# Performance work log

Hardware: AMD Instinct MI355X
Metric: run time of the kernel (lower is better)

The kernel has to match this reference:

```python
import jax, jax.numpy as jnp
import numpy as np

IN_SIZE = 224
KERNEL = 5
STRIDE = 1
IN_CH = 16
OUT_CH = 64
LAMB = 5.0
LR = 0.005
GAMMA = 0.99
EPS_ = 0.01
NH = (IN_SIZE - KERNEL) // STRIDE + 1          # 220 output positions per side
NB_TILES = NH * NH                              # 48400 tiles


def setup_inputs() -> dict:
    key = jax.random.key(0)
    k1, k2 = jax.random.split(key)
    x = jax.random.normal(k1, (1, IN_CH, IN_SIZE, IN_SIZE), dtype=jnp.float32)
    # torch.nn.init.uniform_(param, a=0, b=1)
    W = jax.random.uniform(k2, (OUT_CH, IN_CH, KERNEL, KERNEL), dtype=jnp.float32)
    exp_avg = jnp.zeros((OUT_CH,), dtype=jnp.float32)
    return {"x": x, "W": W, "exp_avg": exp_avg, "clamped": 0}


def _inhibition(out):
    out = jax.nn.relu(out)
    m = jnp.max(out, axis=1, keepdims=True)     # max over channel dim
    out = out / (m + 1e-9)
    return out ** LAMB


def _flatten_input(x):
    # mirrors x.unfold(2,k,s).unfold(3,k,s) -> [T, C*k*k] with (C, kh, kw) ordering
    starts = jnp.arange(NH) * STRIDE
    rows = starts[:, None] + jnp.arange(KERNEL)  # [NH, K]
    p = x[0][:, rows]                            # [C, NH, K, W]
    p = p[:, :, :, rows]                         # [C, NH, K, NH, K]
    p = p.transpose(1, 3, 0, 2, 4)               # [NH, NH, C, K, K]
    return p.reshape(NB_TILES, -1)               # [T, D]


def reference(x, W, exp_avg, clamped):
    # forward conv + inhibition
    out = jax.lax.conv_general_dilated(
        x, W, (STRIDE, STRIDE), 'VALID',
        dimension_numbers=('NCHW', 'OIHW', 'NCHW'))
    out = _inhibition(out)                       # [1, O, NH, NH]

    # Hebbian FullyOrthogonal update (no-grad buffer update in the original)
    y = out[0].transpose(1, 2, 0).reshape(-1, OUT_CH)   # [T, O]
    xf = _flatten_input(x)                               # [T, D]
    Wf = W.reshape(OUT_CH, -1)                           # [O, D]
    # mean_t( lr * (y_t (x) x_t - y_t (x) (y_t W)) ) = lr/T * (Y^T X - (Y^T Y) W)
    yty = y.T @ y                                        # [O, O]
    avg_delta = (LR / NB_TILES) * (y.T @ xf - yty @ Wf)  # [O, D]
    Wnew = jax.nn.relu(Wf + avg_delta).reshape(OUT_CH, IN_CH, KERNEL, KERNEL)
    exp_new = GAMMA * exp_avg + (1.0 - GAMMA) * jnp.mean(y, axis=0)

    # weight decay scaling
    A = exp_new / jnp.mean(exp_new)
    gfp = EPS_ * jnp.tanh(-EPS_ * (A - 1.0)) + 1.0
    gfn = 1.0 / gfp
    pos = jnp.where(Wnew > 0, Wnew, 0.0) * gfp.reshape(-1, 1, 1, 1)
    neg = jnp.where(Wnew < 0, Wnew, 0.0) * gfn.reshape(-1, 1, 1, 1)
    Wfinal = pos + neg
    return out, Wfinal, exp_new
```

## Files before the change

kernel.cpp:

```cpp
#include <hip/hip_runtime.h>
#include <stdint.h>

#define IN_SIZE 224
#define KER 5
#define IN_CH 16
#define OUT_CH 64
#define NH 220
#define NB_TILES (NH * NH)
#define XCH (IN_SIZE * IN_SIZE)
#define OUT_PLANE NB_TILES
#define KP2 51200
#define XS 52224
#define LR_OVER_NB ((float)(0.005 / 48400.0))
#define GAMMA_F 0.99f
#define ONE_MINUS_GAMMA 0.01f
#define EPS_F 0.01f

#define NCHUNK 64
#define CK 800
#define PSTRIDE (64 * 512)

typedef __attribute__((ext_vector_type(8))) short short8;
typedef __attribute__((ext_vector_type(4))) float floatx4;

__device__ inline uint16_t f2bf(float f) {
    uint32_t u = __float_as_uint(f);
    return (uint16_t)((u + 0x7FFFu + ((u >> 16) & 1u)) >> 16);
}
__device__ inline float bf2f(uint16_t h) { return __uint_as_float((uint32_t)h << 16); }

__global__ __launch_bounds__(256) void prepa_kernel(const float* __restrict__ W,
                                                    uint16_t* __restrict__ wrh,
                                                    uint16_t* __restrict__ wrl) {
    int idx = blockIdx.x * 256 + threadIdx.x;
    if (idx >= 13 * 4 * 64 * 8) return;
    int j = idx & 7;
    int lane = (idx >> 3) & 63;
    int ocg = (idx >> 9) & 3;
    int t = idx >> 11;
    int k = (lane >> 4) * 8 + j;
    int s = k >> 4, c = k & 15;
    int oc = 16 * ocg + (lane & 15);
    int tap = 2 * t + s;
    float v = (tap < 25) ? W[oc * 400 + c * 25 + tap] : 0.f;
    uint16_t h = f2bf(v);
    wrh[idx] = h;
    wrl[idx] = f2bf(v - bf2f(h));
}

__global__ __launch_bounds__(256) void conv_prep_kernel(const uint16_t* __restrict__ wrh,
                                                        const uint16_t* __restrict__ wrl,
                                                        float* __restrict__ out,
                                                        uint16_t* __restrict__ yb,
                                                        const float* __restrict__ x,
                                                        uint16_t* __restrict__ xs,
                                                        uint16_t* __restrict__ ones) {
    if (blockIdx.x >= 770) {
        int t = (blockIdx.x - 770) * 256 + threadIdx.x;
        const int perq8 = XS / 8;
        {
            int kj = t / (16 * perq8);
            int rem = t - kj * (16 * perq8);
            int c = rem / perq8;
            int q = (rem - c * perq8) * 8;
            int base = c * XCH;
            uint32_t d[4];
#pragma unroll
            for (int p = 0; p < 4; p++) {
                int i0 = q + kj + 2 * p;
                int i1 = i0 + 1;
                uint16_t h0 = f2bf(x[base + (i0 < XCH ? i0 : XCH - 1)]);
                uint16_t h1 = f2bf(x[base + (i1 < XCH ? i1 : XCH - 1)]);
                d[p] = (uint32_t)h0 | ((uint32_t)h1 << 16);
            }
            *(uint4*)(xs + (kj * 16 + c) * XS + q) = make_uint4(d[0], d[1], d[2], d[3]);
        }
        ushort4 z = {0, 0, 0, 0};
        if (t < 64 * 480) {
            int r = t / 480, q = (t - r * 480) * 4;
            *(ushort4*)(yb + r * KP2 + 49280 + q) = z;
        }
        if (t < 64 * 220) {
            int o = t / 220, i = t - o * 220;
            *(ushort4*)(yb + o * KP2 + i * 224 + 220) = z;
        }
        if (t < 12816) {
            ushort4 o1 = {0x3F80, 0x3F80, 0x3F80, 0x3F80};
            ((ushort4*)ones)[t] = o1;
        }
        return;
    }

    const int lane = threadIdx.x & 63;
    const int w = threadIdx.x >> 6;
    const int l15 = lane & 15;
    const int quad = lane >> 4;
    const int P0 = blockIdx.x * 64;
    const int chalf = quad & 1;
    const int sq = quad >> 1;

    __shared__ uint16_t bsh[5 * 68 * 16];
    __shared__ uint16_t bsl[5 * 68 * 16];
    for (int u = threadIdx.x; u < 680; u += 256) {
        int row = u >> 1;
        int half = u & 1;
        int strip = row / 68;
        int rr = row - strip * 68;
        int grow = P0 + strip * 224 + rr;
        bool inb = grow < XCH;
        uint32_t dh[4], dl[4];
#pragma unroll
        for (int q = 0; q < 4; q++) {
            float v0 = inb ? x[(half * 8 + 2 * q) * XCH + grow] : 0.f;
            float v1 = inb ? x[(half * 8 + 2 * q + 1) * XCH + grow] : 0.f;
            uint16_t h0 = f2bf(v0), h1 = f2bf(v1);
            uint16_t l0 = f2bf(v0 - bf2f(h0)), l1 = f2bf(v1 - bf2f(h1));
            dh[q] = (uint32_t)h0 | ((uint32_t)h1 << 16);
            dl[q] = (uint32_t)l0 | ((uint32_t)l1 << 16);
        }
        int swz = (u ^ ((row >> 2) & 1)) * 8;
        *(uint4*)(bsh + swz) = make_uint4(dh[0], dh[1], dh[2], dh[3]);
        *(uint4*)(bsl + swz) = make_uint4(dl[0], dl[1], dl[2], dl[3]);
    }
    __syncthreads();

    floatx4 acc[4];
#pragma unroll
    for (int g = 0; g < 4; g++) acc[g] = (floatx4){0.f, 0.f, 0.f, 0.f};

#pragma unroll
    for (int t = 0; t < 13; t++) {
        short8 ah = *(const short8*)(wrh + ((t * 4 + w) * 64 + lane) * 8);
        short8 al = *(const short8*)(wrl + ((t * 4 + w) * 64 + lane) * 8);
        const int tap0 = 2 * t, tap1 = 2 * t + 1;
        const int ki0 = tap0 / 5, kj0 = tap0 % 5;
        const int ki1 = (tap1 <= 24) ? tap1 / 5 : 0;
        const int kj1 = (tap1 <= 24) ? tap1 % 5 : 0;
        const int strip = sq ? ki1 : ki0;
        const int kjv = sq ? kj1 : kj0;
#pragma unroll
        for (int g = 0; g < 4; g++) {
            int lrow = strip * 68 + 16 * g + l15 + kjv;
            int unit = lrow * 2 + chalf;
            int off = (unit ^ ((lrow >> 2) & 1)) * 8;
            short8 bh = *(const short8*)(bsh + off);
            short8 bl = *(const short8*)(bsl + off);
            acc[g] = __builtin_amdgcn_mfma_f32_16x16x32_bf16(ah, bh, acc[g], 0, 0, 0);
            acc[g] = __builtin_amdgcn_mfma_f32_16x16x32_bf16(ah, bl, acc[g], 0, 0, 0);
            acc[g] = __builtin_amdgcn_mfma_f32_16x16x32_bf16(al, bh, acc[g], 0, 0, 0);
        }
    }

    __shared__ float wmax[4][64];
    float pmax[4];
#pragma unroll
    for (int g = 0; g < 4; g++) {
        float mx = fmaxf(fmaxf(acc[g][0], acc[g][1]), fmaxf(acc[g][2], acc[g][3]));
        mx = fmaxf(mx, 0.f);
        mx = fmaxf(mx, __shfl_xor(mx, 16));
        mx = fmaxf(mx, __shfl_xor(mx, 32));
        pmax[g] = mx;
    }
    if (quad == 0) {
#pragma unroll
        for (int g = 0; g < 4; g++) wmax[w][g * 16 + l15] = pmax[g];
    }
    __syncthreads();

#pragma unroll
    for (int g = 0; g < 4; g++) {
        int P = P0 + 16 * g + l15;
        int i = P / 224;
        int j = P - i * 224;
        bool valid = j < NH;
        float mx = fmaxf(fmaxf(wmax[0][g * 16 + l15], wmax[1][g * 16 + l15]),
                         fmaxf(wmax[2][g * 16 + l15], wmax[3][g * 16 + l15]));
        float inv = 1.f / (mx + 1e-9f);
#pragma unroll
        for (int r = 0; r < 4; r++) {
            float tv = fmaxf(acc[g][r], 0.f) * inv;
            float t2 = tv * tv;
            tv = t2 * t2 * tv;
            if (valid) {
                int oc = 16 * w + quad * 4 + r;
                out[oc * OUT_PLANE + i * NH + j] = tv;
                yb[oc * KP2 + P] = f2bf(tv);
            }
        }
    }
}

__global__ __launch_bounds__(256) void gemm_kernel(const uint16_t* __restrict__ yb,
                                                   const uint16_t* __restrict__ xs,
                                                   const uint16_t* __restrict__ ones,
                                                   float* __restrict__ Mpart) {
    __shared__ uint16_t As[2][64 * 64];
    __shared__ uint16_t Bs[2][64 * 64];
    const int tid = threadIdx.x;
    const int lane = tid & 63;
    const int w = tid >> 6;
    const int l15 = lane & 15;
    const int quad = lane >> 4;
    const int b = blockIdx.x;
    const int xcd = b & 7;
    const int t8 = b >> 3;
    const int ntile = t8 & 7;
    const int chunk = xcd + 8 * (t8 >> 3);
    const int k0 = chunk * CK;

    const int sr = tid >> 2;
    const int sq = tid & 3;
    const int sseg = sq * 8;
    const uint16_t* pa = yb + sr * KP2 + k0 + sseg;

    int n_g = ntile * 64 + sr;
    const uint16_t* pbase;
    if (n_g < 400) {
        int c = n_g / 25;
        int r = n_g - 25 * c;
        int ki = r / 5;
        int kj = r - 5 * ki;
        pbase = xs + (kj * 16 + c) * XS + ki * 224;
    } else if (n_g < 464) {
        pbase = yb + (n_g - 400) * KP2;
    } else if (n_g == 464) {
        pbase = ones;
    } else {
        pbase = yb;
    }
    const uint16_t* pb = pbase + k0 + sseg;

    const int woff = sr * 64 + ((2 * sq + sr) & 7) * 8;
    const int ru = ((2 * quad + l15) & 7) * 8;
    floatx4 acc[4];
#pragma unroll
    for (int i = 0; i < 4; i++) acc[i] = (floatx4){0.f, 0.f, 0.f, 0.f};

    uint4 ra = *(const uint4*)pa;
    uint4 rb = *(const uint4*)pb;

    for (int s = 0; s < 25; s++) {
        const int p = s & 1;
        *(uint4*)&As[p][woff] = ra;
        *(uint4*)&Bs[p][woff] = rb;
        __syncthreads();
        if (s + 1 < 25) {
            pa += 32;
            pb += 32;
            ra = *(const uint4*)pa;
            rb = *(const uint4*)pb;
        }
        short8 af = *(const short8*)&As[p][(16 * w + l15) * 64 + ru];
#pragma unroll
        for (int ng = 0; ng < 4; ng++) {
            short8 bf = *(const short8*)&Bs[p][(16 * ng + l15) * 64 + ru];
            acc[ng] = __builtin_amdgcn_mfma_f32_16x16x32_bf16(af, bf, acc[ng], 0, 0, 0);
        }
        __syncthreads();
    }

    float* dst = Mpart + chunk * PSTRIDE;
#pragma unroll
    for (int ng = 0; ng < 4; ng++) {
        int col = ntile * 64 + ng * 16 + l15;
        if (col < 465) {
#pragma unroll
            for (int r = 0; r < 4; r++)
                dst[(16 * w + quad * 4 + r) * 512 + col] = acc[ng][r];
        }
    }
}

__global__ __launch_bounds__(256) void finalize_w_kernel(const float* __restrict__ W,
                                                         const float* __restrict__ Mpart,
                                                         const float* __restrict__ exp_avg,
                                                         float* __restrict__ Wout,
                                                         float* __restrict__ expout) {
    __shared__ float gfps[OUT_CH];
    __shared__ float ytys[2][OUT_CH];
    const int tid = threadIdx.x;
    const int bid = blockIdx.x;
    const int first_o = (bid * 256) / 400;

    if (tid < OUT_CH) {
        int o = tid;
        float cs = 0.f;
#pragma unroll 8
        for (int ch = 0; ch < NCHUNK; ch++) cs += Mpart[ch * PSTRIDE + o * 512 + 464];
        float e = GAMMA_F * exp_avg[o] + ONE_MINUS_GAMMA * (cs / (float)NB_TILES);
        float s = e;
        for (int off = 32; off; off >>= 1) s += __shfl_down(s, off);
        s = __shfl(s, 0);
        float A = e / (s / (float)OUT_CH);
        gfps[o] = EPS_F * tanhf(-EPS_F * (A - 1.f)) + 1.f;
        if (bid == 0) expout[o] = e;
    }
    if (tid >= 128) {
        int t = tid - 128;
        int orow = first_o + (t >> 6);
        int k = t & 63;
        float s = 0.f;
        if (orow < OUT_CH) {
#pragma unroll 8
            for (int ch = 0; ch < NCHUNK; ch++) s += Mpart[ch * PSTRIDE + orow * 512 + 400 + k];
        }
        ytys[t >> 6][k] = s;
    }
    __syncthreads();

    int idx = bid * 256 + tid;
    int o = idx / 400;
    int q = idx - o * 400;
    float Mv = 0.f;
#pragma unroll 8
    for (int ch = 0; ch < NCHUNK; ch++) Mv += Mpart[ch * PSTRIDE + o * 512 + q];
    const float* yrow = ytys[o - first_o];
    float dot = 0.f;
#pragma unroll 8
    for (int k = 0; k < OUT_CH; k++) dot = fmaf(yrow[k], W[k * 400 + q], dot);
    float wv = W[idx] + LR_OVER_NB * (Mv - dot);
    wv = fmaxf(wv, 0.f);
    float gp = gfps[o];
    float pos = (wv > 0.f ? wv : 0.f) * gp;
    float neg = (wv < 0.f ? wv : 0.f) / gp;
    Wout[idx] = pos + neg;
}

extern "C" void kernel_launch(void* const* d_in, const int* in_sizes, int n_in,
                              void* d_out, int out_size, void* d_ws, size_t ws_size,
                              hipStream_t stream) {
    const float* x = (const float*)d_in[0];
    const float* W = (const float*)d_in[1];
    const float* exp_avg = (const float*)d_in[2];
    float* out = (float*)d_out;

    float* wsf = (float*)d_ws;
    float* Mpart = wsf + 29760;
    uint16_t* wrh = (uint16_t*)Mpart;
    uint16_t* wrl = wrh + 26624;
    uint16_t* ybf = (uint16_t*)(wsf + 29760 + NCHUNK * PSTRIDE);
    uint16_t* xsb = ybf + OUT_CH * KP2;
    uint16_t* ones = xsb + 5 * 16 * XS;

    float* Wout = out + OUT_CH * OUT_PLANE;
    float* expout = Wout + OUT_CH * IN_CH * KER * KER;

    prepa_kernel<<<104, 256, 0, stream>>>(W, wrh, wrl);
    conv_prep_kernel<<<770 + 2040, 256, 0, stream>>>(wrh, wrl, out, ybf, x, xsb, ones);
    gemm_kernel<<<512, 256, 0, stream>>>(ybf, xsb, ones, Mpart);
    finalize_w_kernel<<<100, 256, 0, stream>>>(W, Mpart, exp_avg, Wout, expout);
}
```

Before: 112.7 us.

## Fuse weight split into conv kernel and atomically reduce GEMM partials

Drops the separate prepa_kernel launch. Each conv block now loads W directly and splits it into bf16 hi/lo register fragments. The GEMM kernel now atomically adds its per-chunk partial sums into one zeroed 64x512 buffer instead of writing 64 partial slabs. The finalize kernel then reads single values instead of summing 64 chunks. This trades one launch and a strided reduction for redundant per-block weight conversion (26 short8 registers per thread) and float atomic contention across 64 chunks.

```diff
diff --git a/kernel.cpp b/kernel.cpp
--- a/kernel.cpp
+++ b/kernel.cpp
@@ -29,32 +29,13 @@
 }
 __device__ inline float bf2f(uint16_t h) { return __uint_as_float((uint32_t)h << 16); }
 
-__global__ __launch_bounds__(256) void prepa_kernel(const float* __restrict__ W,
-                                                    uint16_t* __restrict__ wrh,
-                                                    uint16_t* __restrict__ wrl) {
-    int idx = blockIdx.x * 256 + threadIdx.x;
-    if (idx >= 13 * 4 * 64 * 8) return;
-    int j = idx & 7;
-    int lane = (idx >> 3) & 63;
-    int ocg = (idx >> 9) & 3;
-    int t = idx >> 11;
-    int k = (lane >> 4) * 8 + j;
-    int s = k >> 4, c = k & 15;
-    int oc = 16 * ocg + (lane & 15);
-    int tap = 2 * t + s;
-    float v = (tap < 25) ? W[oc * 400 + c * 25 + tap] : 0.f;
-    uint16_t h = f2bf(v);
-    wrh[idx] = h;
-    wrl[idx] = f2bf(v - bf2f(h));
-}
-
-__global__ __launch_bounds__(256) void conv_prep_kernel(const uint16_t* __restrict__ wrh,
-                                                        const uint16_t* __restrict__ wrl,
+__global__ __launch_bounds__(256) void conv_prep_kernel(const float* __restrict__ W,
                                                         float* __restrict__ out,
                                                         uint16_t* __restrict__ yb,
                                                         const float* __restrict__ x,
                                                         uint16_t* __restrict__ xs,
-                                                        uint16_t* __restrict__ ones) {
+                                                        uint16_t* __restrict__ ones,
+                                                        float* __restrict__ msum) {
     if (blockIdx.x >= 770) {
         int t = (blockIdx.x - 770) * 256 + threadIdx.x;
         const int perq8 = XS / 8;
@@ -88,6 +69,10 @@
             ushort4 o1 = {0x3F80, 0x3F80, 0x3F80, 0x3F80};
             ((ushort4*)ones)[t] = o1;
         }
+        if (t < 8192) {
+            float4 z4 = make_float4(0.f, 0.f, 0.f, 0.f);
+            ((float4*)msum)[t] = z4;
+        }
         return;
     }
 
@@ -98,6 +83,23 @@
     const int P0 = blockIdx.x * 64;
     const int chalf = quad & 1;
     const int sq = quad >> 1;
+
+    const int s_tap = quad >> 1;
+    const float* wbase = W + (16 * w + l15) * 400 + ((quad & 1) * 8) * 25 + s_tap;
+    short8 ahr[13], alr[13];
+#pragma unroll
+    for (int t = 0; t < 13; t++) {
+        const bool dead = (t == 12);
+#pragma unroll
+        for (int j = 0; j < 8; j++) {
+            int off = (dead && s_tap == 1) ? 0 : (j * 25 + 2 * t);
+            float v = wbase[off];
+            if (dead && s_tap == 1) v = 0.f;
+            uint16_t h = f2bf(v);
+            ahr[t][j] = (short)h;
+            alr[t][j] = (short)f2bf(v - bf2f(h));
+        }
+    }
 
     __shared__ uint16_t bsh[5 * 68 * 16];
     __shared__ uint16_t bsl[5 * 68 * 16];
@@ -130,8 +132,8 @@
 
 #pragma unroll
     for (int t = 0; t < 13; t++) {
-        short8 ah = *(const short8*)(wrh + ((t * 4 + w) * 64 + lane) * 8);
-        short8 al = *(const short8*)(wrl + ((t * 4 + w) * 64 + lane) * 8);
+        short8 ah = ahr[t];
+        short8 al = alr[t];
         const int tap0 = 2 * t, tap1 = 2 * t + 1;
         const int ki0 = tap0 / 5, kj0 = tap0 % 5;
         const int ki1 = (tap1 <= 24) ? tap1 / 5 : 0;
@@ -193,7 +195,7 @@
 __global__ __launch_bounds__(256) void gemm_kernel(const uint16_t* __restrict__ yb,
                                                    const uint16_t* __restrict__ xs,
                                                    const uint16_t* __restrict__ ones,
-                                                   float* __restrict__ Mpart) {
+                                                   float* __restrict__ msum) {
     __shared__ uint16_t As[2][64 * 64];
     __shared__ uint16_t Bs[2][64 * 64];
     const int tid = threadIdx.x;
@@ -232,6 +234,7 @@
 
     const int woff = sr * 64 + ((2 * sq + sr) & 7) * 8;
     const int ru = ((2 * quad + l15) & 7) * 8;
+
     floatx4 acc[4];
 #pragma unroll
     for (int i = 0; i < 4; i++) acc[i] = (floatx4){0.f, 0.f, 0.f, 0.f};
@@ -259,20 +262,19 @@
         __syncthreads();
     }
 
-    float* dst = Mpart + chunk * PSTRIDE;
 #pragma unroll
     for (int ng = 0; ng < 4; ng++) {
         int col = ntile * 64 + ng * 16 + l15;
         if (col < 465) {
 #pragma unroll
             for (int r = 0; r < 4; r++)
-                dst[(16 * w + quad * 4 + r) * 512 + col] = acc[ng][r];
+                atomicAdd(&msum[(16 * w + quad * 4 + r) * 512 + col], acc[ng][r]);
         }
     }
 }
 
 __global__ __launch_bounds__(256) void finalize_w_kernel(const float* __restrict__ W,
-                                                         const float* __restrict__ Mpart,
+                                                         const float* __restrict__ msum,
                                                          const float* __restrict__ exp_avg,
                                                          float* __restrict__ Wout,
                                                          float* __restrict__ expout) {
@@ -284,9 +286,7 @@
 
     if (tid < OUT_CH) {
         int o = tid;
-        float cs = 0.f;
-#pragma unroll 8
-        for (int ch = 0; ch < NCHUNK; ch++) cs += Mpart[ch * PSTRIDE + o * 512 + 464];
+        float cs = msum[o * 512 + 464];
         float e = GAMMA_F * exp_avg[o] + ONE_MINUS_GAMMA * (cs / (float)NB_TILES);
         float s = e;
         for (int off = 32; off; off >>= 1) s += __shfl_down(s, off);
@@ -299,11 +299,7 @@
         int t = tid - 128;
         int orow = first_o + (t >> 6);
         int k = t & 63;
-        float s = 0.f;
-        if (orow < OUT_CH) {
-#pragma unroll 8
-            for (int ch = 0; ch < NCHUNK; ch++) s += Mpart[ch * PSTRIDE + orow * 512 + 400 + k];
-        }
+        float s = (orow < OUT_CH) ? msum[orow * 512 + 400 + k] : 0.f;
         ytys[t >> 6][k] = s;
     }
     __syncthreads();
@@ -311,9 +307,7 @@
     int idx = bid * 256 + tid;
     int o = idx / 400;
     int q = idx - o * 400;
-    float Mv = 0.f;
-#pragma unroll 8
-    for (int ch = 0; ch < NCHUNK; ch++) Mv += Mpart[ch * PSTRIDE + o * 512 + q];
+    float Mv = msum[o * 512 + q];
     const float* yrow = ytys[o - first_o];
     float dot = 0.f;
 #pragma unroll 8
@@ -335,9 +329,7 @@
     float* out = (float*)d_out;
 
     float* wsf = (float*)d_ws;
-    float* Mpart = wsf + 29760;
-    uint16_t* wrh = (uint16_t*)Mpart;
-    uint16_t* wrl = wrh + 26624;
+    float* msum = wsf + 29760;
     uint16_t* ybf = (uint16_t*)(wsf + 29760 + NCHUNK * PSTRIDE);
     uint16_t* xsb = ybf + OUT_CH * KP2;
     uint16_t* ones = xsb + 5 * 16 * XS;
@@ -345,8 +337,7 @@
     float* Wout = out + OUT_CH * OUT_PLANE;
     float* expout = Wout + OUT_CH * IN_CH * KER * KER;
 
-    prepa_kernel<<<104, 256, 0, stream>>>(W, wrh, wrl);
-    conv_prep_kernel<<<770 + 2040, 256, 0, stream>>>(wrh, wrl, out, ybf, x, xsb, ones);
-    gemm_kernel<<<512, 256, 0, stream>>>(ybf, xsb, ones, Mpart);
-    finalize_w_kernel<<<100, 256, 0, stream>>>(W, Mpart, exp_avg, Wout, expout);
-}
+    conv_prep_kernel<<<770 + 2040, 256, 0, stream>>>(W, out, ybf, x, xsb, ones, msum);
+    gemm_kernel<<<512, 256, 0, stream>>>(ybf, xsb, ones, msum);
+    finalize_w_kernel<<<100, 256, 0, stream>>>(W, msum, exp_avg, Wout, expout);
+}
```

After: 144.0 us. 27.7% more time.

## Reduce split-K GEMM partials with atomics and pad LDS rows instead of XOR swizzle

Applied to the files above, without the earlier changes.

The GEMM no longer writes 64 per-chunk partial matrices for the finalize kernel to sum. Each block now atomically adds its tile into a single zero-initialised 64x512 accumulator, cleared in the conv_prep kernel. The finalize kernel reads only one value per element instead of looping over 64 chunks. The shared-memory tiles also switch from an XOR swizzle to a padded row stride of 40 elements, which is less shared memory. The trade-offs are float atomic contention from 64 chunks hitting the same addresses, plus a summation order that is no longer deterministic.

```diff
diff --git a/kernel.cpp b/kernel.cpp
--- a/kernel.cpp
+++ b/kernel.cpp
@@ -54,7 +54,8 @@
                                                         uint16_t* __restrict__ yb,
                                                         const float* __restrict__ x,
                                                         uint16_t* __restrict__ xs,
-                                                        uint16_t* __restrict__ ones) {
+                                                        uint16_t* __restrict__ ones,
+                                                        float* __restrict__ msum) {
     if (blockIdx.x >= 770) {
         int t = (blockIdx.x - 770) * 256 + threadIdx.x;
         const int perq8 = XS / 8;
@@ -88,6 +89,10 @@
             ushort4 o1 = {0x3F80, 0x3F80, 0x3F80, 0x3F80};
             ((ushort4*)ones)[t] = o1;
         }
+        if (t < 8192) {
+            float4 z4 = make_float4(0.f, 0.f, 0.f, 0.f);
+            ((float4*)msum)[t] = z4;
+        }
         return;
     }
 
@@ -193,14 +198,15 @@
 __global__ __launch_bounds__(256) void gemm_kernel(const uint16_t* __restrict__ yb,
                                                    const uint16_t* __restrict__ xs,
                                                    const uint16_t* __restrict__ ones,
-                                                   float* __restrict__ Mpart) {
-    __shared__ uint16_t As[2][64 * 64];
-    __shared__ uint16_t Bs[2][64 * 64];
+                                                   float* __restrict__ msum) {
+    __shared__ uint16_t As[2][64 * 40];
+    __shared__ uint16_t Bs[2][64 * 40];
     const int tid = threadIdx.x;
     const int lane = tid & 63;
     const int w = tid >> 6;
     const int l15 = lane & 15;
     const int quad = lane >> 4;
+    const int kg = quad * 8;
     const int b = blockIdx.x;
     const int xcd = b & 7;
     const int t8 = b >> 3;
@@ -209,8 +215,7 @@
     const int k0 = chunk * CK;
 
     const int sr = tid >> 2;
-    const int sq = tid & 3;
-    const int sseg = sq * 8;
+    const int sseg = (tid & 3) * 8;
     const uint16_t* pa = yb + sr * KP2 + k0 + sseg;
 
     int n_g = ntile * 64 + sr;
@@ -230,8 +235,6 @@
     }
     const uint16_t* pb = pbase + k0 + sseg;
 
-    const int woff = sr * 64 + ((2 * sq + sr) & 7) * 8;
-    const int ru = ((2 * quad + l15) & 7) * 8;
     floatx4 acc[4];
 #pragma unroll
     for (int i = 0; i < 4; i++) acc[i] = (floatx4){0.f, 0.f, 0.f, 0.f};
@@ -241,8 +244,8 @@
 
     for (int s = 0; s < 25; s++) {
         const int p = s & 1;
-        *(uint4*)&As[p][woff] = ra;
-        *(uint4*)&Bs[p][woff] = rb;
+        *(uint4*)&As[p][sr * 40 + sseg] = ra;
+        *(uint4*)&Bs[p][sr * 40 + sseg] = rb;
         __syncthreads();
         if (s + 1 < 25) {
             pa += 32;
@@ -250,29 +253,28 @@
             ra = *(const uint4*)pa;
             rb = *(const uint4*)pb;
         }
-        short8 af = *(const short8*)&As[p][(16 * w + l15) * 64 + ru];
+        short8 af = *(const short8*)&As[p][(16 * w + l15) * 40 + kg];
 #pragma unroll
         for (int ng = 0; ng < 4; ng++) {
-            short8 bf = *(const short8*)&Bs[p][(16 * ng + l15) * 64 + ru];
+            short8 bf = *(const short8*)&Bs[p][(16 * ng + l15) * 40 + kg];
             acc[ng] = __builtin_amdgcn_mfma_f32_16x16x32_bf16(af, bf, acc[ng], 0, 0, 0);
         }
         __syncthreads();
     }
 
-    float* dst = Mpart + chunk * PSTRIDE;
 #pragma unroll
     for (int ng = 0; ng < 4; ng++) {
         int col = ntile * 64 + ng * 16 + l15;
         if (col < 465) {
 #pragma unroll
             for (int r = 0; r < 4; r++)
-                dst[(16 * w + quad * 4 + r) * 512 + col] = acc[ng][r];
+                atomicAdd(&msum[(16 * w + quad * 4 + r) * 512 + col], acc[ng][r]);
         }
     }
 }
 
 __global__ __launch_bounds__(256) void finalize_w_kernel(const float* __restrict__ W,
-                                                         const float* __restrict__ Mpart,
+                                                         const float* __restrict__ msum,
                                                          const float* __restrict__ exp_avg,
                                                          float* __restrict__ Wout,
                                                          float* __restrict__ expout) {
@@ -284,9 +286,7 @@
 
     if (tid < OUT_CH) {
         int o = tid;
-        float cs = 0.f;
-#pragma unroll 8
-        for (int ch = 0; ch < NCHUNK; ch++) cs += Mpart[ch * PSTRIDE + o * 512 + 464];
+        float cs = msum[o * 512 + 464];
         float e = GAMMA_F * exp_avg[o] + ONE_MINUS_GAMMA * (cs / (float)NB_TILES);
         float s = e;
         for (int off = 32; off; off >>= 1) s += __shfl_down(s, off);
@@ -299,11 +299,7 @@
         int t = tid - 128;
         int orow = first_o + (t >> 6);
         int k = t & 63;
-        float s = 0.f;
-        if (orow < OUT_CH) {
-#pragma unroll 8
-            for (int ch = 0; ch < NCHUNK; ch++) s += Mpart[ch * PSTRIDE + orow * 512 + 400 + k];
-        }
+        float s = (orow < OUT_CH) ? msum[orow * 512 + 400 + k] : 0.f;
         ytys[t >> 6][k] = s;
     }
     __syncthreads();
@@ -311,9 +307,7 @@
     int idx = bid * 256 + tid;
     int o = idx / 400;
     int q = idx - o * 400;
-    float Mv = 0.f;
-#pragma unroll 8
-    for (int ch = 0; ch < NCHUNK; ch++) Mv += Mpart[ch * PSTRIDE + o * 512 + q];
+    float Mv = msum[o * 512 + q];
     const float* yrow = ytys[o - first_o];
     float dot = 0.f;
 #pragma unroll 8
@@ -335,8 +329,8 @@
     float* out = (float*)d_out;
 
     float* wsf = (float*)d_ws;
-    float* Mpart = wsf + 29760;
-    uint16_t* wrh = (uint16_t*)Mpart;
+    float* msum = wsf + 29760;
+    uint16_t* wrh = (uint16_t*)(wsf + 29760 + 64 * 512);
     uint16_t* wrl = wrh + 26624;
     uint16_t* ybf = (uint16_t*)(wsf + 29760 + NCHUNK * PSTRIDE);
     uint16_t* xsb = ybf + OUT_CH * KP2;
@@ -346,7 +340,7 @@
     float* expout = Wout + OUT_CH * IN_CH * KER * KER;
 
     prepa_kernel<<<104, 256, 0, stream>>>(W, wrh, wrl);
-    conv_prep_kernel<<<770 + 2040, 256, 0, stream>>>(wrh, wrl, out, ybf, x, xsb, ones);
-    gemm_kernel<<<512, 256, 0, stream>>>(ybf, xsb, ones, Mpart);
-    finalize_w_kernel<<<100, 256, 0, stream>>>(W, Mpart, exp_avg, Wout, expout);
-}
+    conv_prep_kernel<<<770 + 2040, 256, 0, stream>>>(wrh, wrl, out, ybf, x, xsb, ones, msum);
+    gemm_kernel<<<512, 256, 0, stream>>>(ybf, xsb, ones, msum);
+    finalize_w_kernel<<<100, 256, 0, stream>>>(W, msum, exp_avg, Wout, expout);
+}
```

Result: faster. 108.9 us (-3.4%).
